# Kernel tuning notes

Measured on AMD Instinct MI355X. Metric: run time of the kernel, lower is better.

## Reference

```python
import jax, jax.numpy as jnp
import numpy as np

B = 100000      # query points
L = 8           # num levels
N_RBF = 256     # RBF centers per level
F = 16          # features per level
OUT = 3         # output dim


def setup_inputs() -> dict:
    key = jax.random.key(0)
    k = jax.random.split(key, 6)
    x = jax.random.normal(k[0], (B, 3), dtype=jnp.float32)
    # small-magnitude features so gaussian RBF responses are non-degenerate
    feats = 0.1 * jax.random.normal(k[1], (B, L * F), dtype=jnp.float32)
    # centers initialized uniform(-1e-4, 1e-4) as in the torch module
    centers = jax.random.uniform(k[2], (L, N_RBF, F), dtype=jnp.float32,
                                 minval=-1e-4, maxval=1e-4)
    # log-width parameters (exp'd in forward); small perturbation around 0
    betas = 0.01 * jax.random.normal(k[3], (L, N_RBF, F), dtype=jnp.float32)
    W = jax.random.normal(k[4], (OUT, N_RBF * L), dtype=jnp.float32) / np.sqrt(N_RBF * L)
    b = jax.random.normal(k[5], (OUT,), dtype=jnp.float32) * 0.01
    return {"x": x, "feats": feats, "centers": centers, "betas": betas, "W": W, "b": b}


def reference(x, feats, centers, betas, W, b):
    # centers, betas: [L, N, F]. x is unused by the original forward (faithful).
    Lnum, N, f = centers.shape
    rbfs = []
    for i in range(Lnum):
        # concat of first i+1 per-level tables along feature axis -> [N, (i+1)*f]
        C = centers[: i + 1].transpose(1, 0, 2).reshape(N, (i + 1) * f)
        Bw = jnp.exp(betas[: i + 1].transpose(1, 0, 2).reshape(N, (i + 1) * f))
        x_in = feats[:, : (i + 1) * f]                      # [B, (i+1)*f]
        term1 = (x_in * x_in) @ Bw.T                        # [B, N]
        term2 = x_in @ (Bw * C).T                           # [B, N]
        term3 = jnp.sum(Bw * C * C, axis=1)                 # [N]
        dist_sq = term1 - 2.0 * term2 + term3[None, :]
        rbfs.append(jnp.exp(-0.5 * dist_sq))                # gaussian basis
    outs = jnp.concatenate(rbfs, axis=-1)                   # [B, L*N]
    return outs @ W.T + b
```

## Files before the change

### kernel.cpp

```cpp
#include <hip/hip_runtime.h>
#include <math.h>

#define LN 8
#define NRBF 256
#define FD 16
#define OUTD 3
#define KC (-0.72134752044f)

typedef __attribute__((ext_vector_type(8))) short short8;
typedef __attribute__((ext_vector_type(4))) float floatx4;
typedef __attribute__((ext_vector_type(2))) float floatx2;

__device__ __forceinline__ short f2bf(float f) {
    unsigned u = __builtin_bit_cast(unsigned, f);
    u += 0x7fffu + ((u >> 16) & 1u);
    return (short)(u >> 16);
}


__global__ __launch_bounds__(256) void prep(
    const float* __restrict__ centers, const float* __restrict__ betas,
    const float* __restrict__ W, short* __restrict__ PKB, float* __restrict__ EPI)
{
    __shared__ float ls[LN * 32];
    int blk = blockIdx.x;
    int tid = threadIdx.x;
    if (blk < 32) {
        int g    = blk * 256 + tid;
        int lane = g & 63;
        int j    = (g >> 6) & 7;
        int nt   = g >> 9;
        int n    = nt * 16 + (lane & 15);
        int kq   = lane >> 4;
        size_t base = ((size_t)(j * NRBF + n)) * FD + kq * 4;
        float4 bq = *(const float4*)(betas + base);
        float4 cq = *(const float4*)(centers + base);
        float a0 = KC * __expf(bq.x), a1 = KC * __expf(bq.y);
        float a2 = KC * __expf(bq.z), a3 = KC * __expf(bq.w);
        short8 v;
        v[0] = f2bf(a0); v[1] = f2bf(-2.0f * a0 * cq.x);
        v[2] = f2bf(a1); v[3] = f2bf(-2.0f * a1 * cq.y);
        v[4] = f2bf(a2); v[5] = f2bf(-2.0f * a2 * cq.z);
        v[6] = f2bf(a3); v[7] = f2bf(-2.0f * a3 * cq.w);
        *((short8*)(PKB + (size_t)g * 8)) = v;
    } else {
        int jj = tid >> 5;
        int nl = tid & 31;
        int n  = (blk - 32) * 32 + nl;
        const float* bp = betas   + ((size_t)(jj * NRBF + n)) * FD;
        const float* cp = centers + ((size_t)(jj * NRBF + n)) * FD;
        float s = 0.f;
#pragma unroll
        for (int q = 0; q < 4; ++q) {
            float4 bq = *(const float4*)(bp + q * 4);
            float4 cq = *(const float4*)(cp + q * 4);
            s = fmaf(__expf(bq.x) * cq.x, cq.x, s);
            s = fmaf(__expf(bq.y) * cq.y, cq.y, s);
            s = fmaf(__expf(bq.z) * cq.z, cq.z, s);
            s = fmaf(__expf(bq.w) * cq.w, cq.w, s);
        }
        ls[jj * 32 + nl] = s;
        __syncthreads();
        float t3 = 0.f;
        for (int j2 = 0; j2 <= jj; ++j2) t3 += ls[j2 * 32 + nl];
        float E = __builtin_amdgcn_exp2f(KC * t3);
        float4 e;
        e.x = W[0 * (LN * NRBF) + jj * NRBF + n] * E;
        e.y = W[1 * (LN * NRBF) + jj * NRBF + n] * E;
        e.z = W[2 * (LN * NRBF) + jj * NRBF + n] * E;
        e.w = 0.f;
        ((float4*)EPI)[((size_t)(n >> 4) * 128) + jj * 16 + (n & 15)] = e;
    }
}

#define CVT(dst, vv)  do {                                         \
        short8 f_;                                                 \
        f_[0] = f2bf((vv).x * (vv).x); f_[1] = f2bf((vv).x);       \
        f_[2] = f2bf((vv).y * (vv).y); f_[3] = f2bf((vv).y);       \
        f_[4] = f2bf((vv).z * (vv).z); f_[5] = f2bf((vv).z);       \
        f_[6] = f2bf((vv).w * (vv).w); f_[7] = f2bf((vv).w);       \
        (dst) = f_; } while (0)

__global__ __launch_bounds__(256) void rbf_mfma(
    const float* __restrict__ feats, const short* __restrict__ PKB,
    const float* __restrict__ EPI, const float* __restrict__ bias,
    float* __restrict__ out, int B)
{
    int tid  = threadIdx.x;
    int lane = tid & 63;
    int w    = tid >> 6;
    int ntile = (B + 15) >> 4;
    int tile = blockIdx.x * 4 + w;
    bool tvalid = (tile < ntile);
    if (!tvalid) tile = ntile - 1;
    int b0 = tile * 16;
    int m  = lane & 15;
    int kq = lane >> 4;
    int brow = b0 + m; if (brow >= B) brow = B - 1;
    const float* xrow = feats + (size_t)brow * (LN * FD) + kq * 4;

    const short8* pkb8 = (const short8*)PKB;
    const float4* epi4 = (const float4*)EPI;

#define EXPPROJ(accv, ev)                                          \
    do {                                                           \
        floatx2 exy_ = { (ev).x, (ev).y };                         \
        floatx2 ezz_ = { (ev).z, (ev).z };                         \
        float rv0_ = __builtin_amdgcn_exp2f((accv)[0]);            \
        float rv1_ = __builtin_amdgcn_exp2f((accv)[1]);            \
        float rv2_ = __builtin_amdgcn_exp2f((accv)[2]);            \
        float rv3_ = __builtin_amdgcn_exp2f((accv)[3]);            \
        o01[0] += (floatx2){rv0_, rv0_} * exy_;                    \
        o01[1] += (floatx2){rv1_, rv1_} * exy_;                    \
        o01[2] += (floatx2){rv2_, rv2_} * exy_;                    \
        o01[3] += (floatx2){rv3_, rv3_} * exy_;                    \
        oz[0]  += (floatx2){rv0_, rv1_} * ezz_;                    \
        oz[1]  += (floatx2){rv2_, rv3_} * ezz_;                    \
    } while (0)

    short8 af[LN];
#pragma unroll
    for (int j = 0; j < LN; ++j) {
        float4 xa = *(const float4*)(xrow + j * FD);
        CVT(af[j], xa);
    }

    floatx2 o01[4];
    floatx2 oz[2];
#pragma unroll
    for (int r = 0; r < 4; ++r) o01[r] = (floatx2){0.f, 0.f};
    oz[0] = (floatx2){0.f, 0.f}; oz[1] = (floatx2){0.f, 0.f};

#pragma unroll 1
    for (int nt = 0; nt < 16; ++nt) {
        const short8* pb = pkb8 + (size_t)nt * 512 + lane;
        const float4* eb = epi4 + (size_t)nt * 128 + m;

        floatx4 acc = (floatx4){0.f, 0.f, 0.f, 0.f};
        floatx4 accp;

#pragma unroll
        for (int j = 0; j < LN; ++j) {
            short8 bf = pb[j * 64];
            acc = __builtin_amdgcn_mfma_f32_16x16x32_bf16(af[j], bf, acc, 0, 0, 0);
            if (j > 0) {
                float4 e = eb[(j - 1) * 16];
                EXPPROJ(accp, e);
            }
            accp = acc;
        }
        {
            float4 e = eb[7 * 16];
            EXPPROJ(accp, e);
        }
    }
#undef EXPPROJ

    float oacc[12];
#pragma unroll
    for (int r = 0; r < 4; ++r) {
        oacc[r * 3 + 0] = o01[r].x;
        oacc[r * 3 + 1] = o01[r].y;
        oacc[r * 3 + 2] = (r & 1) ? oz[r >> 1].y : oz[r >> 1].x;
    }
#pragma unroll
    for (int i = 0; i < 12; ++i) {
        oacc[i] += __shfl_xor(oacc[i], 1);
        oacc[i] += __shfl_xor(oacc[i], 2);
        oacc[i] += __shfl_xor(oacc[i], 4);
        oacc[i] += __shfl_xor(oacc[i], 8);
    }

    if (tvalid && m < OUTD) {
        float bv = bias[m];
#pragma unroll
        for (int r = 0; r < 4; ++r) {
            int row = b0 + kq * 4 + r;
            if (row < B) out[(size_t)row * OUTD + m] = oacc[r * 3 + m] + bv;
        }
    }
}

extern "C" void kernel_launch(void* const* d_in, const int* in_sizes, int n_in,
                              void* d_out, int out_size, void* d_ws, size_t ws_size,
                              hipStream_t stream) {
    const float* feats   = (const float*)d_in[1];
    const float* centers = (const float*)d_in[2];
    const float* betas   = (const float*)d_in[3];
    const float* W       = (const float*)d_in[4];
    const float* bias    = (const float*)d_in[5];
    float* out = (float*)d_out;
    int B = in_sizes[1] / (LN * FD);

    short* PKB = (short*)d_ws;
    float* EPI = (float*)((char*)d_ws + 65536 * 2);

    prep<<<40, 256, 0, stream>>>(centers, betas, W, PKB, EPI);

    int tiles  = (B + 15) / 16;
    int blocks = (tiles + 3) / 4;
    rbf_mfma<<<blocks, 256, 0, stream>>>(feats, PKB, EPI, bias, out, B);
}
```

Measured before the change: 148.9 us.

## Stage RBF weight tables through double-buffered LDS with async global-to-LDS loads

After: 140.2 us. -5.8%, faster.

```diff
diff --git a/kernel.cpp b/kernel.cpp
--- a/kernel.cpp
+++ b/kernel.cpp
@@ -86,6 +86,9 @@
     const float* __restrict__ EPI, const float* __restrict__ bias,
     float* __restrict__ out, int B)
 {
+    __shared__ short8 pk_s[2][1024];
+    __shared__ float4 ep_s[2][256];
+
     int tid  = threadIdx.x;
     int lane = tid & 63;
     int w    = tid >> 6;
@@ -99,8 +102,22 @@
     int brow = b0 + m; if (brow >= B) brow = B - 1;
     const float* xrow = feats + (size_t)brow * (LN * FD) + kq * 4;
 
-    const short8* pkb8 = (const short8*)PKB;
-    const float4* epi4 = (const float4*)EPI;
+#define STAGE(buf, c)                                                           \
+    do {                                                                        \
+        _Pragma("unroll")                                                       \
+        for (int i = 0; i < 4; ++i) {                                           \
+            const short* gp = PKB + ((size_t)(c) * 1024 + (w * 4 + i) * 64 + lane) * 8; \
+            __builtin_amdgcn_global_load_lds(                                   \
+                (const __attribute__((address_space(1))) void*)gp,              \
+                (__attribute__((address_space(3))) void*)&pk_s[buf][(w * 4 + i) * 64], \
+                16, 0, 0);                                                      \
+        }                                                                       \
+        const float* ge = EPI + ((size_t)(c) * 256 + w * 64 + lane) * 4;        \
+        __builtin_amdgcn_global_load_lds(                                       \
+            (const __attribute__((address_space(1))) void*)ge,                  \
+            (__attribute__((address_space(3))) void*)&ep_s[buf][w * 64],        \
+            16, 0, 0);                                                          \
+    } while (0)
 
 #define EXPPROJ(accv, ev)                                          \
     do {                                                           \
@@ -118,6 +135,8 @@
         oz[1]  += (floatx2){rv2_, rv3_} * ezz_;                    \
     } while (0)
 
+    STAGE(0, 0);
+
     short8 af[LN];
 #pragma unroll
     for (int j = 0; j < LN; ++j) {
@@ -131,29 +150,41 @@
     for (int r = 0; r < 4; ++r) o01[r] = (floatx2){0.f, 0.f};
     oz[0] = (floatx2){0.f, 0.f}; oz[1] = (floatx2){0.f, 0.f};
 
+    __syncthreads();
+
 #pragma unroll 1
-    for (int nt = 0; nt < 16; ++nt) {
-        const short8* pb = pkb8 + (size_t)nt * 512 + lane;
-        const float4* eb = epi4 + (size_t)nt * 128 + m;
-
-        floatx4 acc = (floatx4){0.f, 0.f, 0.f, 0.f};
-        floatx4 accp;
+    for (int c = 0; c < 8; ++c) {
+        int cur = c & 1;
+        if (c < 7) STAGE(cur ^ 1, c + 1);
+
+        floatx4 accA = (floatx4){0.f, 0.f, 0.f, 0.f};
+        floatx4 accB = (floatx4){0.f, 0.f, 0.f, 0.f};
+        floatx4 accpA, accpB;
 
 #pragma unroll
         for (int j = 0; j < LN; ++j) {
-            short8 bf = pb[j * 64];
-            acc = __builtin_amdgcn_mfma_f32_16x16x32_bf16(af[j], bf, acc, 0, 0, 0);
+            short8 bfA = pk_s[cur][j * 64 + lane];
+            short8 bfB = pk_s[cur][512 + j * 64 + lane];
+            accA = __builtin_amdgcn_mfma_f32_16x16x32_bf16(af[j], bfA, accA, 0, 0, 0);
+            accB = __builtin_amdgcn_mfma_f32_16x16x32_bf16(af[j], bfB, accB, 0, 0, 0);
             if (j > 0) {
-                float4 e = eb[(j - 1) * 16];
-                EXPPROJ(accp, e);
+                float4 eA = ep_s[cur][(j - 1) * 16 + m];
+                EXPPROJ(accpA, eA);
+                float4 eB = ep_s[cur][128 + (j - 1) * 16 + m];
+                EXPPROJ(accpB, eB);
             }
-            accp = acc;
+            accpA = accA;
+            accpB = accB;
         }
         {
-            float4 e = eb[7 * 16];
-            EXPPROJ(accp, e);
-        }
-    }
+            float4 eA = ep_s[cur][7 * 16 + m];
+            EXPPROJ(accpA, eA);
+            float4 eB = ep_s[cur][128 + 7 * 16 + m];
+            EXPPROJ(accpB, eB);
+        }
+        __syncthreads();
+    }
+#undef STAGE
 #undef EXPPROJ
 
     float oacc[12];
```
